# Optimization experiments

Measured on AMD Instinct MI355X. Metric: run time of the kernel, lower is better.

## Reference

```python
import jax, jax.numpy as jnp
import numpy as np

T, B, D = 1024, 64, 256   # time, batch, input dim
L, DC = 1024, 256         # context length, context dim
H, A = 256, 256           # hidden, attention dim
NEG = -1e9


def setup_inputs() -> dict:
    key = jax.random.key(0)
    ks = jax.random.split(key, 12)
    s = lambda fan: 1.0 / np.sqrt(fan)
    inp = {
        'x': jax.random.normal(ks[0], (T, B, D), jnp.float32),
        'lengths': jnp.maximum(jax.random.randint(ks[1], (B,), 1, T + 1), 1).astype(jnp.int32),
        'context': jax.random.normal(ks[2], (B, L, DC), jnp.float32),
        'ctx_lengths': jnp.maximum(jax.random.randint(ks[3], (B,), 1, L + 1), 1).astype(jnp.int32),
        'Wc': jax.random.normal(ks[4], (DC, A), jnp.float32) * s(DC),
        'Wx': jax.random.normal(ks[5], (D, A), jnp.float32) * s(D),
        'Wh': jax.random.normal(ks[6], (H, A), jnp.float32) * s(H),
        'v': jax.random.normal(ks[7], (A,), jnp.float32) * s(A),
        'W_ih': jax.random.normal(ks[8], (D + DC, 3 * H), jnp.float32) * s(D + DC),
        'W_hh': jax.random.normal(ks[9], (H, 3 * H), jnp.float32) * s(H),
        'b_ih': jnp.zeros((3 * H,), jnp.float32),
        'b_hh': jnp.zeros((3 * H,), jnp.float32),
    }
    return inp


def reference(x, lengths, context, ctx_lengths, Wc, Wx, Wh, v, W_ih, W_hh, b_ih, b_hh):
    # Precompute context projection once (shared across all timesteps). [B, L, A]
    ctx_proj = jnp.einsum('bld,da->bla', context, Wc)
    ctx_mask = jnp.arange(L)[None, :] < ctx_lengths[:, None]  # [B, L]
    h0 = jnp.zeros((B, H), x.dtype)

    def step(h, inputs):
        xt, t = inputs  # xt: [B, D]
        # Additive attention over the context.
        e = jnp.tanh(ctx_proj + (xt @ Wx)[:, None, :] + (h @ Wh)[:, None, :])  # [B, L, A]
        scores = jnp.where(ctx_mask, jnp.einsum('bla,a->bl', e, v), NEG)
        alpha = jax.nn.softmax(scores, axis=-1)                  # [B, L]
        c = jnp.einsum('bl,bld->bd', alpha, context)             # [B, DC]
        # GRU over [x_t ; c_t].
        z = jnp.concatenate([xt, c], axis=-1)                    # [B, D+DC]
        gi = z @ W_ih + b_ih
        gh = h @ W_hh + b_hh
        r = jax.nn.sigmoid(gi[:, :H] + gh[:, :H])
        u = jax.nn.sigmoid(gi[:, H:2 * H] + gh[:, H:2 * H])
        n = jnp.tanh(gi[:, 2 * H:] + r * gh[:, 2 * H:])
        h_new = u * h + (1.0 - u) * n
        valid = (t < lengths)[:, None]                           # ragged masking
        h_next = jnp.where(valid, h_new, h)
        out = jnp.where(valid, h_new, 0.0)
        return h_next, out

    h_final, outputs = jax.lax.scan(step, h0, (x, jnp.arange(T)))
    return outputs, h_final[None]  # [T, B, H], [num_layers=1, B, H]
```

## Files before the change

### kernel.cpp

```cpp
#include <hip/hip_runtime.h>
#include <cstddef>

#define T_ 1024
#define B_ 64
#define D_ 256
#define L_ 1024
#define DC_ 256
#define H_ 256
#define A_ 256
#define G3 768
#define LQ 256
#define NBLK 4

typedef unsigned int uint2v __attribute__((ext_vector_type(2)));
typedef float float4v __attribute__((ext_vector_type(4)));
typedef float float2v __attribute__((ext_vector_type(2)));
typedef unsigned short ushort4v __attribute__((ext_vector_type(4)));

__device__ __forceinline__ float bflo(unsigned int w) { return __uint_as_float(w << 16); }
__device__ __forceinline__ float bfhi(unsigned int w) { return __uint_as_float(w & 0xffff0000u); }
__device__ __forceinline__ unsigned short f2bf(float f) {
  unsigned int x = __float_as_uint(f);
  return (unsigned short)((x + 0x7fffu + ((x >> 16) & 1u)) >> 16);
}
__device__ __forceinline__ float fast_tanh(float xx) {
  float e = __expf(2.0f * xx);
  return 1.0f - 2.0f / (e + 1.0f);
}
__device__ __forceinline__ float sigmoidf_(float xx) {
  return 1.0f / (1.0f + __expf(-xx));
}
__device__ __forceinline__ void st_agent_f(float* p, float v) {
  __hip_atomic_store(p, v, __ATOMIC_RELAXED, __HIP_MEMORY_SCOPE_AGENT);
}
__device__ __forceinline__ float ld_agent_f(const float* p) {
  return __hip_atomic_load(p, __ATOMIC_RELAXED, __HIP_MEMORY_SCOPE_AGENT);
}
__device__ __forceinline__ void group_arrive(unsigned int* ctrb) {
  __syncthreads();
  if (threadIdx.x == 0) {
    __hip_atomic_fetch_add(ctrb, 1u, __ATOMIC_RELAXED, __HIP_MEMORY_SCOPE_AGENT);
  }
}
__device__ __forceinline__ void group_wait(unsigned int* ctrb, unsigned int target) {
  if (threadIdx.x == 0) {
    while (__hip_atomic_load(ctrb, __ATOMIC_RELAXED, __HIP_MEMORY_SCOPE_AGENT) < target) {
      __builtin_amdgcn_s_sleep(2);
    }
  }
  __syncthreads();
}

__global__ void f2bf_kernel(const float* __restrict__ src,
                            unsigned short* __restrict__ dst, int n) {
  int i = (blockIdx.x * blockDim.x + threadIdx.x) * 4;
  if (i < n) {
    float4 v = *(const float4*)(src + i);
    ushort4 o;
    o.x = f2bf(v.x); o.y = f2bf(v.y); o.z = f2bf(v.z); o.w = f2bf(v.w);
    *(ushort4*)(dst + i) = o;
  }
}

__global__ void pack_wih_kernel(const float* __restrict__ W_ih,
                                unsigned short* __restrict__ dst) {
  int idx = blockIdx.x * 256 + threadIdx.x;
  int kb = idx / (512 * 192);
  int rem = idx % (512 * 192);
  int r = rem / 192, jg = rem % 192;
  int g = jg >> 6, jj = jg & 63;
  int j = g * 256 + kb * 64 + jj;
  dst[idx] = f2bf(W_ih[(size_t)r * G3 + j]);
}
__global__ void pack_whh_kernel(const float* __restrict__ W_hh,
                                unsigned short* __restrict__ dst) {
  int idx = blockIdx.x * 256 + threadIdx.x;
  int kb = idx / (256 * 192);
  int rem = idx % (256 * 192);
  int r = rem / 192, jg = rem % 192;
  int g = jg >> 6, jj = jg & 63;
  int j = g * 256 + kb * 64 + jj;
  dst[idx] = f2bf(W_hh[(size_t)r * G3 + j]);
}

__global__ __launch_bounds__(1024) void encoder_kernel(
    const float* __restrict__ x, const int* __restrict__ lengths,
    const float* __restrict__ context, const int* __restrict__ ctx_lengths,
    const float* __restrict__ Wc,
    const unsigned short* __restrict__ wx_b, const unsigned short* __restrict__ wh_b,
    const float* __restrict__ v,
    const unsigned short* __restrict__ wih_pk, const unsigned short* __restrict__ whh_pk,
    const float* __restrict__ b_ih, const float* __restrict__ b_hh,
    const unsigned short* __restrict__ ctx_bf, float* __restrict__ out,
    float* __restrict__ cpart, float* __restrict__ hx, unsigned int* __restrict__ ctr) {
  __shared__ __align__(16) unsigned short ctx_lds[A_ * LQ];
  __shared__ __align__(16) float scratch[4096];
  __shared__ __align__(16) float xt_s[D_];
  __shared__ __align__(16) float h_s[H_];
  __shared__ __align__(16) float c_s[DC_];
  __shared__ float2 qv_s[A_];
  __shared__ float pv_s[LQ];
  __shared__ float gatI[192], gatH[192];
  __shared__ float bsl_i[192], bsl_h[192];
  __shared__ float wsum_l[4];

  const int gb = blockIdx.x;
  const int b = gb >> 2, kb = gb & 3;
  const int tid = threadIdx.x;
  const int len = lengths[b];
  const int clen = ctx_lengths[b];
  const int lbase = kb * LQ;
  const float* ctxb = context + (size_t)b * L_ * DC_;
  const unsigned short* ctxbf_b = ctx_bf + (size_t)b * L_ * DC_;
  const unsigned short* wihp = wih_pk + (size_t)kb * (512 * 192);
  const unsigned short* whhp = whh_pk + (size_t)kb * (256 * 192);
  float* cpart_grp = cpart + (size_t)b * NBLK * 264;
  float* cpart_my = cpart_grp + kb * 264;
  float* hx_b = hx + (size_t)b * 256;
  unsigned int* ctr_b = ctr + b * 32;

  const int p16 = tid >> 6, i64 = tid & 63;
  const int pq = tid / 96, jc = tid % 96;

  if (tid < 256) { h_s[tid] = 0.0f; qv_s[tid] = make_float2(0.0f, v[tid]); }
  if (tid < 192) {
    int g = tid >> 6, jj = tid & 63;
    int j = g * 256 + kb * 64 + jj;
    bsl_i[tid] = b_ih[j]; bsl_h[tid] = b_hh[j];
  }
  __syncthreads();

  {
    const int a = tid & 255, lq4 = tid >> 8;
    for (int tl = 0; tl < 16; ++tl) {
      for (int idx = tid; idx < 4096; idx += 1024) {
        int r = idx >> 8, d = idx & 255;
        scratch[d * 16 + r] = ctxb[(size_t)(lbase + tl * 16 + r) * DC_ + d];
      }
      __syncthreads();
      float a0 = 0.f, a1 = 0.f, a2 = 0.f, a3 = 0.f;
#pragma unroll 4
      for (int d = 0; d < 256; ++d) {
        float w = Wc[(size_t)d * A_ + a];
        const float* ps = &scratch[d * 16 + lq4 * 4];
        a0 += ps[0] * w; a1 += ps[1] * w; a2 += ps[2] * w; a3 += ps[3] * w;
      }
      int l0 = tl * 16 + lq4 * 4;
      ushort4v o; o.x = f2bf(a0); o.y = f2bf(a1); o.z = f2bf(a2); o.w = f2bf(a3);
      *(ushort4v*)&ctx_lds[a * LQ + l0] = o;
      __syncthreads();
    }
  }

  for (int t = 0; t < len; ++t) {
    if (tid < 64) {
      *(float4v*)&xt_s[tid * 4] =
          *(const float4v*)&x[((size_t)t * B_ + b) * D_ + tid * 4];
    }
    __syncthreads();

    {
      const int a0 = i64 * 4, k0 = p16 * 16;
      float4v acc = {0.f, 0.f, 0.f, 0.f};
#pragma unroll
      for (int k = k0; k < k0 + 16; ++k) {
        float xv = xt_s[k];
        uint2v w = *(const uint2v*)(wx_b + (size_t)k * A_ + a0);
        acc.x += xv * bflo(w.x); acc.y += xv * bfhi(w.x);
        acc.z += xv * bflo(w.y); acc.w += xv * bfhi(w.y);
      }
#pragma unroll
      for (int k = k0; k < k0 + 16; ++k) {
        float hv = h_s[k];
        uint2v w = *(const uint2v*)(wh_b + (size_t)k * A_ + a0);
        acc.x += hv * bflo(w.x); acc.y += hv * bfhi(w.x);
        acc.z += hv * bflo(w.y); acc.w += hv * bfhi(w.y);
      }
      *(float4v*)&scratch[tid * 4] = acc;
    }
    __syncthreads();
    if (tid < 256) {
      float q = 0.f;
#pragma unroll
      for (int p = 0; p < 16; ++p) q += scratch[p * 256 + tid];
      qv_s[tid].x = q;
    }
    __syncthreads();

    uint2v cstage[16];
#pragma unroll
    for (int i = 0; i < 16; ++i) {
      cstage[i] = *(const uint2v*)(ctxbf_b + (size_t)(lbase + p16 * 16 + i) * DC_ + i64 * 4);
    }

    {
      const int ll0 = i64 * 4;
      float4v acc = {0.f, 0.f, 0.f, 0.f};
      if (lbase + ll0 < clen) {
        const unsigned short* basep = ctx_lds + p16 * 16 * LQ + ll0;
#pragma unroll 4
        for (int aa = 0; aa < 16; ++aa) {
          uint2v w = *(const uint2v*)(basep + aa * LQ);
          float2 qv = qv_s[p16 * 16 + aa];
          acc.x += qv.y * fast_tanh(bflo(w.x) + qv.x);
          acc.y += qv.y * fast_tanh(bfhi(w.x) + qv.x);
          acc.z += qv.y * fast_tanh(bflo(w.y) + qv.x);
          acc.w += qv.y * fast_tanh(bfhi(w.y) + qv.x);
        }
      }
      *(float4v*)&scratch[tid * 4] = acc;
    }
    __syncthreads();
    if (tid < 256) {
      float s = 0.f;
#pragma unroll
      for (int p = 0; p < 16; ++p) s += scratch[p * 256 + tid];
      int lg = lbase + tid;
      float e = (lg < clen) ? __expf(s) : 0.f;
      pv_s[tid] = e;
      float sm = e;
#pragma unroll
      for (int off = 32; off; off >>= 1) sm += __shfl_xor(sm, off);
      if ((tid & 63) == 0) wsum_l[tid >> 6] = sm;
    }
    __syncthreads();

    {
      float4v acc = {0.f, 0.f, 0.f, 0.f};
#pragma unroll
      for (int i = 0; i < 16; ++i) {
        float pv = pv_s[p16 * 16 + i];
        uint2v w = cstage[i];
        acc.x += pv * bflo(w.x); acc.y += pv * bfhi(w.x);
        acc.z += pv * bflo(w.y); acc.w += pv * bfhi(w.y);
      }
      *(float4v*)&scratch[tid * 4] = acc;
    }
    __syncthreads();
    if (tid < 256) {
      float cp = 0.f;
#pragma unroll
      for (int p = 0; p < 16; ++p) cp += scratch[p * 256 + tid];
      st_agent_f(&cpart_my[tid], cp);
    }
    if (tid == 0) {
      st_agent_f(&cpart_my[256], wsum_l[0] + wsum_l[1] + wsum_l[2] + wsum_l[3]);
    }
    group_arrive(ctr_b);

    if (tid < 768) {
      const int r0 = pq * 32;
      float a0 = 0.f, a1 = 0.f, h0 = 0.f, h1 = 0.f;
#pragma unroll 8
      for (int i = 0; i < 32; ++i) {
        float zk = xt_s[r0 + i];
        unsigned int wi = *(const unsigned int*)(wihp + (size_t)(r0 + i) * 192 + 2 * jc);
        a0 += zk * bflo(wi); a1 += zk * bfhi(wi);
        float hv = h_s[r0 + i];
        unsigned int wh = *(const unsigned int*)(whhp + (size_t)(r0 + i) * 192 + 2 * jc);
        h0 += hv * bflo(wh); h1 += hv * bfhi(wh);
      }
      *(float2v*)&scratch[pq * 192 + 2 * jc] = float2v{a0, a1};
      *(float2v*)&scratch[1536 + pq * 192 + 2 * jc] = float2v{h0, h1};
    }
    __syncthreads();
    if (tid < 192) {
      float gi = bsl_i[tid], gh = bsl_h[tid];
#pragma unroll
      for (int p = 0; p < 8; ++p) {
        gi += scratch[p * 192 + tid];
        gh += scratch[1536 + p * 192 + tid];
      }
      gatI[tid] = gi; gatH[tid] = gh;
    }
    group_wait(ctr_b, 8u * t + 4u);

    {
      float cc = 0.f;
      if (tid < 256) {
#pragma unroll
        for (int k2 = 0; k2 < 4; ++k2) cc += ld_agent_f(cpart_grp + k2 * 264 + tid);
      } else if (tid < 260) {
        wsum_l[tid - 256] = ld_agent_f(cpart_grp + (tid - 256) * 264 + 256);
      }
      __syncthreads();
      if (tid < 256) {
        c_s[tid] = cc / (wsum_l[0] + wsum_l[1] + wsum_l[2] + wsum_l[3]);
      }
    }
    __syncthreads();

    if (tid < 768) {
      const int r0 = pq * 32;
      float b0 = 0.f, b1 = 0.f;
#pragma unroll 8
      for (int i = 0; i < 32; ++i) {
        float zk = c_s[r0 + i];
        unsigned int wi =
            *(const unsigned int*)(wihp + (size_t)(256 + r0 + i) * 192 + 2 * jc);
        b0 += zk * bflo(wi); b1 += zk * bfhi(wi);
      }
      *(float2v*)&scratch[pq * 192 + 2 * jc] = float2v{b0, b1};
    }
    __syncthreads();
    if (tid < 192) {
      float gi = gatI[tid];
#pragma unroll
      for (int p = 0; p < 8; ++p) gi += scratch[p * 192 + tid];
      gatI[tid] = gi;
    }
    __syncthreads();
    if (tid < 64) {
      float r = sigmoidf_(gatI[tid] + gatH[tid]);
      float u = sigmoidf_(gatI[64 + tid] + gatH[64 + tid]);
      float n = fast_tanh(gatI[128 + tid] + r * gatH[128 + tid]);
      float hn = u * h_s[kb * 64 + tid] + (1.0f - u) * n;
      st_agent_f(&hx_b[kb * 64 + tid], hn);
      __builtin_nontemporal_store(hn, &out[((size_t)t * B_ + b) * H_ + kb * 64 + tid]);
    }
    group_arrive(ctr_b);
    group_wait(ctr_b, 8u * t + 8u);
    if (tid < 256) h_s[tid] = ld_agent_f(&hx_b[tid]);
    __syncthreads();
  }

  {
    const int n = (T_ - len) * 64;
    for (int idx = tid; idx < n; idx += 1024) {
      int tt = len + (idx >> 6);
      int ii = idx & 63;
      __builtin_nontemporal_store(0.0f, &out[((size_t)tt * B_ + b) * H_ + kb * 64 + ii]);
    }
  }
  if (tid < 64) {
    out[(size_t)T_ * B_ * H_ + (size_t)b * H_ + kb * 64 + tid] = h_s[kb * 64 + tid];
  }
}

extern "C" void kernel_launch(void* const* d_in, const int* in_sizes, int n_in,
                              void* d_out, int out_size, void* d_ws, size_t ws_size,
                              hipStream_t stream) {
  const float* x = (const float*)d_in[0];
  const int* lengths = (const int*)d_in[1];
  const float* context = (const float*)d_in[2];
  const int* ctx_lengths = (const int*)d_in[3];
  const float* Wc = (const float*)d_in[4];
  const float* Wx = (const float*)d_in[5];
  const float* Wh = (const float*)d_in[6];
  const float* v = (const float*)d_in[7];
  const float* W_ih = (const float*)d_in[8];
  const float* W_hh = (const float*)d_in[9];
  const float* b_ih = (const float*)d_in[10];
  const float* b_hh = (const float*)d_in[11];
  float* out = (float*)d_out;

  char* w = (char*)d_ws;
  unsigned short* ctx_bf = (unsigned short*)w;
  unsigned short* wx_b = (unsigned short*)(w + 33554432);
  unsigned short* wh_b = (unsigned short*)(w + 33685504);
  unsigned short* wih_pk = (unsigned short*)(w + 33816576);
  unsigned short* whh_pk = (unsigned short*)(w + 34603008);
  float* cpart = (float*)(w + 34996224);
  float* hx = (float*)(w + 35266560);
  unsigned int* ctr = (unsigned int*)(w + 35332096);

  hipMemsetAsync(ctr, 0, 8192, stream);
  hipLaunchKernelGGL(f2bf_kernel, dim3(16384), dim3(256), 0, stream,
                     context, ctx_bf, B_ * L_ * DC_);
  hipLaunchKernelGGL(f2bf_kernel, dim3(64), dim3(256), 0, stream, Wx, wx_b, D_ * A_);
  hipLaunchKernelGGL(f2bf_kernel, dim3(64), dim3(256), 0, stream, Wh, wh_b, H_ * A_);
  hipLaunchKernelGGL(pack_wih_kernel, dim3(1536), dim3(256), 0, stream, W_ih, wih_pk);
  hipLaunchKernelGGL(pack_whh_kernel, dim3(768), dim3(256), 0, stream, W_hh, whh_pk);
  hipLaunchKernelGGL(encoder_kernel, dim3(B_ * NBLK), dim3(1024), 0, stream,
                     x, lengths, context, ctx_lengths, Wc, wx_b, wh_b, v,
                     wih_pk, whh_pk, b_ih, b_hh, ctx_bf, out, cpart, hx, ctr);
}
```

Baseline: 54.64 ms.

## Compute full GRU gates redundantly per block to drop second group barrier

Each of the four blocks per batch row now computes all 768 GRU gate columns redundantly instead of a 192-column slice. It keeps the full hidden state locally, which removes the hidden-state exchange through global memory and the second cross-block barrier per timestep. The context partials are double-buffered by timestep parity so a single barrier per step is safe. The context-weighted sum now loads bf16 context on demand and skips rows beyond the context length, and v is held in registers. In exchange, each block does four times the gate matvec work and reads the full weight matrices every step.

```diff
diff --git a/kernel.cpp b/kernel.cpp
--- a/kernel.cpp
+++ b/kernel.cpp
@@ -62,46 +62,24 @@
   }
 }
 
-__global__ void pack_wih_kernel(const float* __restrict__ W_ih,
-                                unsigned short* __restrict__ dst) {
-  int idx = blockIdx.x * 256 + threadIdx.x;
-  int kb = idx / (512 * 192);
-  int rem = idx % (512 * 192);
-  int r = rem / 192, jg = rem % 192;
-  int g = jg >> 6, jj = jg & 63;
-  int j = g * 256 + kb * 64 + jj;
-  dst[idx] = f2bf(W_ih[(size_t)r * G3 + j]);
-}
-__global__ void pack_whh_kernel(const float* __restrict__ W_hh,
-                                unsigned short* __restrict__ dst) {
-  int idx = blockIdx.x * 256 + threadIdx.x;
-  int kb = idx / (256 * 192);
-  int rem = idx % (256 * 192);
-  int r = rem / 192, jg = rem % 192;
-  int g = jg >> 6, jj = jg & 63;
-  int j = g * 256 + kb * 64 + jj;
-  dst[idx] = f2bf(W_hh[(size_t)r * G3 + j]);
-}
-
 __global__ __launch_bounds__(1024) void encoder_kernel(
     const float* __restrict__ x, const int* __restrict__ lengths,
     const float* __restrict__ context, const int* __restrict__ ctx_lengths,
     const float* __restrict__ Wc,
     const unsigned short* __restrict__ wx_b, const unsigned short* __restrict__ wh_b,
     const float* __restrict__ v,
-    const unsigned short* __restrict__ wih_pk, const unsigned short* __restrict__ whh_pk,
+    const unsigned short* __restrict__ wih_b, const unsigned short* __restrict__ whh_b,
     const float* __restrict__ b_ih, const float* __restrict__ b_hh,
     const unsigned short* __restrict__ ctx_bf, float* __restrict__ out,
-    float* __restrict__ cpart, float* __restrict__ hx, unsigned int* __restrict__ ctr) {
+    float* __restrict__ cpart, unsigned int* __restrict__ ctr) {
   __shared__ __align__(16) unsigned short ctx_lds[A_ * LQ];
   __shared__ __align__(16) float scratch[4096];
   __shared__ __align__(16) float xt_s[D_];
   __shared__ __align__(16) float h_s[H_];
   __shared__ __align__(16) float c_s[DC_];
-  __shared__ float2 qv_s[A_];
+  __shared__ float q_s[A_];
   __shared__ float pv_s[LQ];
-  __shared__ float gatI[192], gatH[192];
-  __shared__ float bsl_i[192], bsl_h[192];
+  __shared__ float gatI[G3], gatH[G3];
   __shared__ float wsum_l[4];
 
   const int gb = blockIdx.x;
@@ -112,22 +90,19 @@
   const int lbase = kb * LQ;
   const float* ctxb = context + (size_t)b * L_ * DC_;
   const unsigned short* ctxbf_b = ctx_bf + (size_t)b * L_ * DC_;
-  const unsigned short* wihp = wih_pk + (size_t)kb * (512 * 192);
-  const unsigned short* whhp = whh_pk + (size_t)kb * (256 * 192);
-  float* cpart_grp = cpart + (size_t)b * NBLK * 264;
-  float* cpart_my = cpart_grp + kb * 264;
-  float* hx_b = hx + (size_t)b * 256;
+  float* cpart_b = cpart + (size_t)b * 2 * NBLK * 264;
   unsigned int* ctr_b = ctr + b * 32;
 
   const int p16 = tid >> 6, i64 = tid & 63;
-  const int pq = tid / 96, jc = tid % 96;
-
-  if (tid < 256) { h_s[tid] = 0.0f; qv_s[tid] = make_float2(0.0f, v[tid]); }
-  if (tid < 192) {
-    int g = tid >> 6, jj = tid & 63;
-    int j = g * 256 + kb * 64 + jj;
-    bsl_i[tid] = b_ih[j]; bsl_h[tid] = b_hh[j];
-  }
+  const int kq2 = (tid >= 384) ? 1 : 0;
+  const int cj384 = tid - kq2 * 384;
+
+  if (tid < 256) { h_s[tid] = 0.0f; q_s[tid] = 0.0f; }
+  float vreg[16];
+#pragma unroll
+  for (int i = 0; i < 16; ++i) vreg[i] = v[p16 * 16 + i];
+  float breg_i = 0.f, breg_h = 0.f;
+  if (tid < G3) { breg_i = b_ih[tid]; breg_h = b_hh[tid]; }
   __syncthreads();
 
   {
@@ -153,6 +128,9 @@
   }
 
   for (int t = 0; t < len; ++t) {
+    float* cpart_par = cpart_b + (size_t)(t & 1) * NBLK * 264;
+    float* cpart_my = cpart_par + kb * 264;
+
     if (tid < 64) {
       *(float4v*)&xt_s[tid * 4] =
           *(const float4v*)&x[((size_t)t * B_ + b) * D_ + tid * 4];
@@ -183,15 +161,9 @@
       float q = 0.f;
 #pragma unroll
       for (int p = 0; p < 16; ++p) q += scratch[p * 256 + tid];
-      qv_s[tid].x = q;
-    }
-    __syncthreads();
-
-    uint2v cstage[16];
-#pragma unroll
-    for (int i = 0; i < 16; ++i) {
-      cstage[i] = *(const uint2v*)(ctxbf_b + (size_t)(lbase + p16 * 16 + i) * DC_ + i64 * 4);
-    }
+      q_s[tid] = q;
+    }
+    __syncthreads();
 
     {
       const int ll0 = i64 * 4;
@@ -201,11 +173,12 @@
 #pragma unroll 4
         for (int aa = 0; aa < 16; ++aa) {
           uint2v w = *(const uint2v*)(basep + aa * LQ);
-          float2 qv = qv_s[p16 * 16 + aa];
-          acc.x += qv.y * fast_tanh(bflo(w.x) + qv.x);
-          acc.y += qv.y * fast_tanh(bfhi(w.x) + qv.x);
-          acc.z += qv.y * fast_tanh(bflo(w.y) + qv.x);
-          acc.w += qv.y * fast_tanh(bfhi(w.y) + qv.x);
+          float q = q_s[p16 * 16 + aa];
+          float vv = vreg[aa];
+          acc.x += vv * fast_tanh(bflo(w.x) + q);
+          acc.y += vv * fast_tanh(bfhi(w.x) + q);
+          acc.z += vv * fast_tanh(bflo(w.y) + q);
+          acc.w += vv * fast_tanh(bfhi(w.y) + q);
         }
       }
       *(float4v*)&scratch[tid * 4] = acc;
@@ -226,11 +199,13 @@
     __syncthreads();
 
     {
+      const int d0 = i64 * 4;
+      const int lmax = min(LQ, max(0, clen - lbase));
+      const int l0 = p16 * 16, l1 = min(l0 + 16, lmax);
       float4v acc = {0.f, 0.f, 0.f, 0.f};
-#pragma unroll
-      for (int i = 0; i < 16; ++i) {
-        float pv = pv_s[p16 * 16 + i];
-        uint2v w = cstage[i];
+      for (int l = l0; l < l1; ++l) {
+        float pv = pv_s[l];
+        uint2v w = *(const uint2v*)(ctxbf_b + (size_t)(lbase + l) * DC_ + d0);
         acc.x += pv * bflo(w.x); acc.y += pv * bfhi(w.x);
         acc.z += pv * bflo(w.y); acc.w += pv * bfhi(w.y);
       }
@@ -249,39 +224,34 @@
     group_arrive(ctr_b);
 
     if (tid < 768) {
-      const int r0 = pq * 32;
+      const int r0 = kq2 * 128;
       float a0 = 0.f, a1 = 0.f, h0 = 0.f, h1 = 0.f;
 #pragma unroll 8
-      for (int i = 0; i < 32; ++i) {
+      for (int i = 0; i < 128; ++i) {
         float zk = xt_s[r0 + i];
-        unsigned int wi = *(const unsigned int*)(wihp + (size_t)(r0 + i) * 192 + 2 * jc);
+        unsigned int wi = *(const unsigned int*)(wih_b + (size_t)(r0 + i) * G3 + 2 * cj384);
         a0 += zk * bflo(wi); a1 += zk * bfhi(wi);
         float hv = h_s[r0 + i];
-        unsigned int wh = *(const unsigned int*)(whhp + (size_t)(r0 + i) * 192 + 2 * jc);
+        unsigned int wh = *(const unsigned int*)(whh_b + (size_t)(r0 + i) * G3 + 2 * cj384);
         h0 += hv * bflo(wh); h1 += hv * bfhi(wh);
       }
-      *(float2v*)&scratch[pq * 192 + 2 * jc] = float2v{a0, a1};
-      *(float2v*)&scratch[1536 + pq * 192 + 2 * jc] = float2v{h0, h1};
-    }
-    __syncthreads();
-    if (tid < 192) {
-      float gi = bsl_i[tid], gh = bsl_h[tid];
-#pragma unroll
-      for (int p = 0; p < 8; ++p) {
-        gi += scratch[p * 192 + tid];
-        gh += scratch[1536 + p * 192 + tid];
-      }
-      gatI[tid] = gi; gatH[tid] = gh;
-    }
-    group_wait(ctr_b, 8u * t + 4u);
+      *(float2v*)&scratch[kq2 * 768 + 2 * cj384] = float2v{a0, a1};
+      *(float2v*)&scratch[1536 + kq2 * 768 + 2 * cj384] = float2v{h0, h1};
+    }
+    __syncthreads();
+    if (tid < G3) {
+      gatI[tid] = breg_i + scratch[tid] + scratch[768 + tid];
+      gatH[tid] = breg_h + scratch[1536 + tid] + scratch[1536 + 768 + tid];
+    }
+    group_wait(ctr_b, 4u * t + 4u);
 
     {
       float cc = 0.f;
       if (tid < 256) {
 #pragma unroll
-        for (int k2 = 0; k2 < 4; ++k2) cc += ld_agent_f(cpart_grp + k2 * 264 + tid);
+        for (int k2 = 0; k2 < 4; ++k2) cc += ld_agent_f(cpart_par + k2 * 264 + tid);
       } else if (tid < 260) {
-        wsum_l[tid - 256] = ld_agent_f(cpart_grp + (tid - 256) * 264 + 256);
+        wsum_l[tid - 256] = ld_agent_f(cpart_par + (tid - 256) * 264 + 256);
       }
       __syncthreads();
       if (tid < 256) {
@@ -291,36 +261,33 @@
     __syncthreads();
 
     if (tid < 768) {
-      const int r0 = pq * 32;
+      const int r0 = kq2 * 128;
       float b0 = 0.f, b1 = 0.f;
 #pragma unroll 8
-      for (int i = 0; i < 32; ++i) {
+      for (int i = 0; i < 128; ++i) {
         float zk = c_s[r0 + i];
         unsigned int wi =
-            *(const unsigned int*)(wihp + (size_t)(256 + r0 + i) * 192 + 2 * jc);
+            *(const unsigned int*)(wih_b + (size_t)(256 + r0 + i) * G3 + 2 * cj384);
         b0 += zk * bflo(wi); b1 += zk * bfhi(wi);
       }
-      *(float2v*)&scratch[pq * 192 + 2 * jc] = float2v{b0, b1};
-    }
-    __syncthreads();
-    if (tid < 192) {
-      float gi = gatI[tid];
-#pragma unroll
-      for (int p = 0; p < 8; ++p) gi += scratch[p * 192 + tid];
-      gatI[tid] = gi;
-    }
-    __syncthreads();
-    if (tid < 64) {
+      *(float2v*)&scratch[kq2 * 768 + 2 * cj384] = float2v{b0, b1};
+    }
+    __syncthreads();
+    if (tid < G3) {
+      gatI[tid] += scratch[tid] + scratch[768 + tid];
+    }
+    __syncthreads();
+
+    if (tid < 256) {
       float r = sigmoidf_(gatI[tid] + gatH[tid]);
-      float u = sigmoidf_(gatI[64 + tid] + gatH[64 + tid]);
-      float n = fast_tanh(gatI[128 + tid] + r * gatH[128 + tid]);
-      float hn = u * h_s[kb * 64 + tid] + (1.0f - u) * n;
-      st_agent_f(&hx_b[kb * 64 + tid], hn);
-      __builtin_nontemporal_store(hn, &out[((size_t)t * B_ + b) * H_ + kb * 64 + tid]);
-    }
-    group_arrive(ctr_b);
-    group_wait(ctr_b, 8u * t + 8u);
-    if (tid < 256) h_s[tid] = ld_agent_f(&hx_b[tid]);
+      float u = sigmoidf_(gatI[256 + tid] + gatH[256 + tid]);
+      float n = fast_tanh(gatI[512 + tid] + r * gatH[512 + tid]);
+      float hn = u * h_s[tid] + (1.0f - u) * n;
+      h_s[tid] = hn;
+      if ((tid >> 6) == kb) {
+        __builtin_nontemporal_store(hn, &out[((size_t)t * B_ + b) * H_ + tid]);
+      }
+    }
     __syncthreads();
   }
 
@@ -358,20 +325,21 @@
   unsigned short* ctx_bf = (unsigned short*)w;
   unsigned short* wx_b = (unsigned short*)(w + 33554432);
   unsigned short* wh_b = (unsigned short*)(w + 33685504);
-  unsigned short* wih_pk = (unsigned short*)(w + 33816576);
-  unsigned short* whh_pk = (unsigned short*)(w + 34603008);
+  unsigned short* wih_b = (unsigned short*)(w + 33816576);
+  unsigned short* whh_b = (unsigned short*)(w + 34603008);
   float* cpart = (float*)(w + 34996224);
-  float* hx = (float*)(w + 35266560);
-  unsigned int* ctr = (unsigned int*)(w + 35332096);
+  unsigned int* ctr = (unsigned int*)(w + 35536896);
 
   hipMemsetAsync(ctr, 0, 8192, stream);
   hipLaunchKernelGGL(f2bf_kernel, dim3(16384), dim3(256), 0, stream,
                      context, ctx_bf, B_ * L_ * DC_);
   hipLaunchKernelGGL(f2bf_kernel, dim3(64), dim3(256), 0, stream, Wx, wx_b, D_ * A_);
   hipLaunchKernelGGL(f2bf_kernel, dim3(64), dim3(256), 0, stream, Wh, wh_b, H_ * A_);
-  hipLaunchKernelGGL(pack_wih_kernel, dim3(1536), dim3(256), 0, stream, W_ih, wih_pk);
-  hipLaunchKernelGGL(pack_whh_kernel, dim3(768), dim3(256), 0, stream, W_hh, whh_pk);
+  hipLaunchKernelGGL(f2bf_kernel, dim3(384), dim3(256), 0, stream,
+                     W_ih, wih_b, (D_ + DC_) * G3);
+  hipLaunchKernelGGL(f2bf_kernel, dim3(192), dim3(256), 0, stream,
+                     W_hh, whh_b, H_ * G3);
   hipLaunchKernelGGL(encoder_kernel, dim3(B_ * NBLK), dim3(1024), 0, stream,
                      x, lengths, context, ctx_lengths, Wc, wx_b, wh_b, v,
-                     wih_pk, whh_pk, b_ih, b_hh, ctx_bf, out, cpart, hx, ctr);
-}
+                     wih_b, whh_b, b_ih, b_hh, ctx_bf, out, cpart, ctr);
+}
```

Measured after the change: 97.89 ms. 79.2% more time.
